# Optimization experiments

Hardware: AMD Instinct MI355X
Metric: run time of the kernel (lower is better)

## Reference

```python
import jax, jax.numpy as jnp
import numpy as np


def setup_inputs() -> dict:
    key = jax.random.key(0)
    k1, k2, k3, k4, k5 = jax.random.split(key, 5)
    B, L, H = 32, 2048, 768
    in1 = jax.random.normal(k1, (B, H), dtype=jnp.float32)
    in2 = jax.random.normal(k2, (B, H), dtype=jnp.float32)
    text = jax.random.normal(k3, (B, L, H), dtype=jnp.float32)
    textmask = jnp.ones((B, L), dtype=jnp.float32)  # 1 = valid token
    # learned params (nn.Linear weights are [out, in]); small scale avoids tanh saturation
    W2 = jax.random.normal(k4, (H, 3 * H), dtype=jnp.float32) * 0.02
    b2 = jnp.zeros((H,), dtype=jnp.float32)
    W1 = jax.random.normal(k5, (1, H), dtype=jnp.float32) * 0.02
    b1 = jnp.zeros((1,), dtype=jnp.float32)
    return {"in1": in1, "in2": in2, "text": text, "textmask": textmask,
            "W2": W2, "b2": b2, "W1": W1, "b1": b1}


def reference(in1, in2, text, textmask, W2, b2, W1, b1):
    H = in1.shape[-1]
    # Split linear2 weight along input dim instead of materializing cat([in1,in2,text]).
    # Same math: cat @ W2.T == in1@W2a.T + in2@W2b.T + text@W2c.T
    W2a, W2b, W2c = W2[:, :H], W2[:, H:2 * H], W2[:, 2 * H:]
    bias_bh = in1 @ W2a.T + in2 @ W2b.T + b2          # [B, H], broadcast over L
    h = jnp.tanh(jnp.einsum('blh,gh->blg', text, W2c) + bias_bh[:, None, :])  # [B, L, H]
    att = jnp.einsum('blh,h->bl', h, W1[0]) + b1[0]   # [B, L]
    att = jax.nn.softmax((1.0 - textmask) * (-1e20) + att, axis=-1)  # masked softmax [B, L]
    context = jnp.einsum('bl,blh->bh', att, text)     # weighted sum [B, H]
    return context, att[:, None, :]                   # matches (context, att[B,1,L])
```

## Files before the change

### kernel.cpp

```cpp
#include <hip/hip_runtime.h>
#include <hip/hip_bf16.h>

typedef __bf16 bf16x8 __attribute__((ext_vector_type(8)));
typedef __bf16 bf16x4 __attribute__((ext_vector_type(4)));
typedef float  f32x4  __attribute__((ext_vector_type(4)));

#define H 768
#define LSEQ 2048
#define BATCH 32
#define MROWS (BATCH*LSEQ)
#define NT 6
#define W2S 2304

__device__ __forceinline__ void gload_lds16(const void* g, void* l){
  __builtin_amdgcn_global_load_lds((const __attribute__((address_space(1))) void*)g,
                                   (__attribute__((address_space(3))) void*)l, 16, 0, 0);
}

__global__ void w2c_cvt_k(const float* __restrict__ W2, __bf16* __restrict__ w2cb){
  int i4 = blockIdx.x*256 + threadIdx.x;
  int g  = i4 / 192;
  int hc = (i4 % 192) * 4;
  f32x4 v = *(const f32x4*)(W2 + (size_t)g*W2S + 1536 + hc);
  bf16x4 o; o[0]=(__bf16)v[0]; o[1]=(__bf16)v[1]; o[2]=(__bf16)v[2]; o[3]=(__bf16)v[3];
  *(bf16x4*)(w2cb + (size_t)g*H + hc) = o;
}

__global__ void bias_k(const float* __restrict__ in1, const float* __restrict__ in2,
                       const float* __restrict__ W2, const float* __restrict__ b2,
                       float* __restrict__ bias){
  int b = blockIdx.y;
  int g = blockIdx.x*64 + (threadIdx.x & 63);
  int q = threadIdx.x >> 6;
  const float* wa = W2 + (size_t)g*W2S + q*192;
  const float* wb = wa + H;
  const float* x1 = in1 + b*H + q*192;
  const float* x2 = in2 + b*H + q*192;
  float acc = 0.f;
  #pragma unroll 8
  for (int h=0; h<192; h+=4){
    f32x4 a4 = *(const f32x4*)(wa+h);
    f32x4 c4 = *(const f32x4*)(x1+h);
    f32x4 b4 = *(const f32x4*)(wb+h);
    f32x4 d4 = *(const f32x4*)(x2+h);
    acc += a4[0]*c4[0]+a4[1]*c4[1]+a4[2]*c4[2]+a4[3]*c4[3];
    acc += b4[0]*d4[0]+b4[1]*d4[1]+b4[2]*d4[2]+b4[3]*d4[3];
  }
  __shared__ float sm[4][64];
  sm[q][threadIdx.x&63] = acc;
  __syncthreads();
  if (q==0){
    float r = sm[0][threadIdx.x]+sm[1][threadIdx.x]+sm[2][threadIdx.x]+sm[3][threadIdx.x] + b2[g];
    bias[(size_t)b*H + g] = r;
  }
}

__global__ __launch_bounds__(256,3) void fused_gemm_att_k(
    const float* __restrict__ text, const __bf16* __restrict__ w2cb,
    const float* __restrict__ bias, const float* __restrict__ W1,
    float* __restrict__ attp)
{
  __shared__ __align__(16) __bf16 a_lds[2][128*32];
  __shared__ __align__(16) __bf16 b_lds[2][128*32];
  __shared__ float att_lds[2][128];

  int bid = blockIdx.x;
  int lin = (bid & 7)*384 + (bid >> 3);
  int mt  = lin / 6;
  int nt  = lin % 6;
  int m0  = mt << 7;
  int b   = m0 >> 11;
  int t = threadIdx.x, lane = t & 63, wid = t >> 6;
  int wm = wid >> 1, wn = wid & 1;
  int fr = lane & 15, fc = lane >> 4;

  const float*  atile = text + (size_t)m0*H;
  const __bf16* btile = w2cb + (size_t)(nt*128)*H;

  f32x4 acc[4][4];
  #pragma unroll
  for (int mi=0;mi<4;++mi)
    #pragma unroll
    for (int ni=0;ni<4;++ni) acc[mi][ni] = (f32x4){0.f,0.f,0.f,0.f};

  int arow = t>>1, ahalf = t&1;
  const float* aptr = atile + (size_t)arow*H + ahalf*16;
  int awOff[2];
  #pragma unroll
  for (int j=0;j<2;++j) awOff[j] = arow*32 + ((2*ahalf + j) ^ ((arow>>1)&3))*8;
  f32x4 aReg[4];

  const __bf16* bsrc[2];
  int bdst[2];
  #pragma unroll
  for (int j=0;j<2;++j){
    int slot = wid*2 + j;
    int n = slot*16 + (lane>>2);
    bsrc[j] = btile + (size_t)n*H + ((lane&3)^((n>>1)&3))*8;
    bdst[j] = slot*512 + lane*8;
  }

  int offA[4], offB[4];
  #pragma unroll
  for (int i=0;i<4;++i){
    int row = wm*64 + i*16 + fr;
    offA[i] = row*32 + ((fc ^ ((row>>1)&3))*8);
    int n = wn*64 + i*16 + fr;
    offB[i] = n*32 + ((fc ^ ((n>>1)&3))*8);
  }

  auto loadA = [&](int kk){
    #pragma unroll
    for (int j=0;j<4;++j) aReg[j] = *(const f32x4*)(aptr + kk*32 + j*4);
  };
  auto writeA = [&](int bf){
    #pragma unroll
    for (int j=0;j<2;++j){
      bf16x8 v;
      v[0]=(__bf16)aReg[2*j][0]; v[1]=(__bf16)aReg[2*j][1];
      v[2]=(__bf16)aReg[2*j][2]; v[3]=(__bf16)aReg[2*j][3];
      v[4]=(__bf16)aReg[2*j+1][0]; v[5]=(__bf16)aReg[2*j+1][1];
      v[6]=(__bf16)aReg[2*j+1][2]; v[7]=(__bf16)aReg[2*j+1][3];
      *(bf16x8*)&a_lds[bf][awOff[j]] = v;
    }
  };
  auto stageB = [&](int bf, int kk){
    #pragma unroll
    for (int j=0;j<2;++j)
      gload_lds16(bsrc[j] + kk*32, &b_lds[bf][bdst[j]]);
  };
  auto compute = [&](int bf){
    bf16x8 af[4], bq[4];
    #pragma unroll
    for (int i=0;i<4;++i){
      af[i] = *(const bf16x8*)&a_lds[bf][offA[i]];
      bq[i] = *(const bf16x8*)&b_lds[bf][offB[i]];
    }
    __builtin_amdgcn_s_setprio(1);
    #pragma unroll
    for (int mi=0;mi<4;++mi)
      #pragma unroll
      for (int ni=0;ni<4;++ni)
        acc[mi][ni] = __builtin_amdgcn_mfma_f32_16x16x32_bf16(af[mi], bq[ni], acc[mi][ni], 0,0,0);
    __builtin_amdgcn_s_setprio(0);
  };

  loadA(0);
  writeA(0);
  stageB(0, 0);
  loadA(1);
  asm volatile("s_waitcnt vmcnt(0) lgkmcnt(0)" ::: "memory");
  __builtin_amdgcn_s_barrier();

  #pragma unroll 2
  for (int kk=0; kk<22; ++kk){
    int cur = kk&1, nxt = cur^1;
    stageB(nxt, kk+1);
    writeA(nxt);
    loadA(kk+2);
    compute(cur);
    asm volatile("s_waitcnt vmcnt(4) lgkmcnt(0)" ::: "memory");
    __builtin_amdgcn_sched_barrier(0);
    __builtin_amdgcn_s_barrier();
    __builtin_amdgcn_sched_barrier(0);
  }
  {
    stageB(1, 23);
    writeA(1);
    compute(0);
    asm volatile("s_waitcnt vmcnt(0) lgkmcnt(0)" ::: "memory");
    __builtin_amdgcn_sched_barrier(0);
    __builtin_amdgcn_s_barrier();
    __builtin_amdgcn_sched_barrier(0);
  }
  compute(1);

  float bb[4], ww[4];
  int gb = nt*128 + wn*64 + fr;
  #pragma unroll
  for (int ni=0;ni<4;++ni){ bb[ni]=bias[(size_t)b*H + gb + ni*16]; ww[ni]=W1[gb + ni*16]; }

  float av[16];
  #pragma unroll
  for (int mi=0;mi<4;++mi)
    #pragma unroll
    for (int r=0;r<4;++r){
      float s = 0.f;
      #pragma unroll
      for (int ni=0;ni<4;++ni){
        float x = acc[mi][ni][r] + bb[ni];
        float e = __expf(2.0f*x);
        s += ww[ni] * ((e-1.0f)*__builtin_amdgcn_rcpf(e+1.0f));
      }
      av[mi*4+r] = s;
    }
  #pragma unroll
  for (int off=1; off<16; off<<=1)
    #pragma unroll
    for (int i=0;i<16;++i) av[i] += __shfl_xor(av[i], off);

  if (fr==0){
    #pragma unroll
    for (int mi=0;mi<4;++mi)
      #pragma unroll
      for (int r=0;r<4;++r)
        att_lds[wn][wm*64 + mi*16 + fc*4 + r] = av[mi*4+r];
  }
  __syncthreads();
  if (t < 128) attp[(size_t)nt*MROWS + m0 + t] = att_lds[0][t] + att_lds[1][t];
}

__global__ void softmax_k(const float* __restrict__ attp, const float* __restrict__ tmask,
                          const float* __restrict__ b1, float* __restrict__ att){
  int b = blockIdx.x, t = threadIdx.x;
  int lane = t & 63, wv = t >> 6;
  __shared__ float sl[LSEQ];
  __shared__ float red[4];
  float b1v = b1[0];
  float lmax = -3.0e38f;
  for (int i=t; i<LSEQ; i+=256){
    float v = b1v;
    #pragma unroll
    for (int p=0;p<NT;++p) v += attp[(size_t)p*MROWS + b*LSEQ + i];
    v += (1.0f - tmask[b*LSEQ+i]) * -1.0e20f;
    sl[i] = v;
    lmax = fmaxf(lmax, v);
  }
  #pragma unroll
  for (int off=32; off>=1; off>>=1) lmax = fmaxf(lmax, __shfl_xor(lmax, off));
  if (lane==0) red[wv] = lmax;
  __syncthreads();
  float mx = fmaxf(fmaxf(red[0],red[1]), fmaxf(red[2],red[3]));
  __syncthreads();
  float lsum = 0.f;
  for (int i=t; i<LSEQ; i+=256){
    float e = __expf(sl[i]-mx);
    sl[i] = e;
    lsum += e;
  }
  #pragma unroll
  for (int off=32; off>=1; off>>=1) lsum += __shfl_xor(lsum, off);
  if (lane==0) red[wv] = lsum;
  __syncthreads();
  float inv = 1.0f/(red[0]+red[1]+red[2]+red[3]);
  for (int i=t; i<LSEQ; i+=256) att[(size_t)b*LSEQ+i] = sl[i]*inv;
}

__global__ void ctxpart_k(const float* __restrict__ text, const float* __restrict__ att,
                          float* __restrict__ ctxp){
  int chunk = blockIdx.x, b = blockIdx.y, t = threadIdx.x;
  const float* tp = text + ((size_t)(b*LSEQ + chunk*64))*H + 4*t;
  const float* ap = att + (size_t)b*LSEQ + chunk*64;
  f32x4 acc = {0.f,0.f,0.f,0.f};
  #pragma unroll 4
  for (int l=0;l<64;++l){
    float a = ap[l];
    f32x4 v = *(const f32x4*)(tp + (size_t)l*H);
    acc[0] += a*v[0]; acc[1] += a*v[1]; acc[2] += a*v[2]; acc[3] += a*v[3];
  }
  *(f32x4*)(ctxp + ((size_t)(b*32+chunk))*H + 4*t) = acc;
}

__global__ void ctxred_k(const float* __restrict__ ctxp, float* __restrict__ out){
  int b = blockIdx.x, h = threadIdx.x;
  float s = 0.f;
  #pragma unroll 8
  for (int c=0;c<32;++c) s += ctxp[((size_t)(b*32+c))*H + h];
  out[(size_t)b*H + h] = s;
}

extern "C" void kernel_launch(void* const* d_in, const int* in_sizes, int n_in,
                              void* d_out, int out_size, void* d_ws, size_t ws_size,
                              hipStream_t stream){
  (void)in_sizes; (void)n_in; (void)out_size; (void)ws_size;
  const float* in1   = (const float*)d_in[0];
  const float* in2   = (const float*)d_in[1];
  const float* text  = (const float*)d_in[2];
  const float* tmask = (const float*)d_in[3];
  const float* W2    = (const float*)d_in[4];
  const float* b2    = (const float*)d_in[5];
  const float* W1    = (const float*)d_in[6];
  const float* b1    = (const float*)d_in[7];
  float* out = (float*)d_out;
  char*  ws  = (char*)d_ws;
  __bf16* w2cb = (__bf16*)(ws);
  float* biasb = (float*)(ws + 1179648);
  float* attp  = (float*)(ws + 1277952);
  float* ctxp  = (float*)(ws + 2850816);
  float* att_out = out + BATCH*H;

  w2c_cvt_k      <<<dim3(576),   dim3(256), 0, stream>>>(W2, w2cb);
  bias_k         <<<dim3(12,32), dim3(256), 0, stream>>>(in1, in2, W2, b2, biasb);
  fused_gemm_att_k<<<dim3(3072), dim3(256), 0, stream>>>(text, w2cb, biasb, W1, attp);
  softmax_k      <<<dim3(32),    dim3(256), 0, stream>>>(attp, tmask, b1, att_out);
  ctxpart_k      <<<dim3(32,32), dim3(192), 0, stream>>>(text, att_out, ctxp);
  ctxred_k       <<<dim3(32),    dim3(768), 0, stream>>>(ctxp, out);
}
```

Baseline: 205.8 us.

## Pre-convert text to bf16 and stage both GEMM operands via direct LDS loads

```diff
diff --git a/kernel.cpp b/kernel.cpp
--- a/kernel.cpp
+++ b/kernel.cpp
@@ -24,6 +24,15 @@
   f32x4 v = *(const f32x4*)(W2 + (size_t)g*W2S + 1536 + hc);
   bf16x4 o; o[0]=(__bf16)v[0]; o[1]=(__bf16)v[1]; o[2]=(__bf16)v[2]; o[3]=(__bf16)v[3];
   *(bf16x4*)(w2cb + (size_t)g*H + hc) = o;
+}
+
+__global__ void text_cvt_k(const float* __restrict__ in, __bf16* __restrict__ outb){
+  const size_t N4 = (size_t)MROWS*H/4;
+  for (size_t i = blockIdx.x*256 + threadIdx.x; i < N4; i += (size_t)2048*256){
+    f32x4 v = ((const f32x4*)in)[i];
+    bf16x4 o; o[0]=(__bf16)v[0]; o[1]=(__bf16)v[1]; o[2]=(__bf16)v[2]; o[3]=(__bf16)v[3];
+    ((bf16x4*)outb)[i] = o;
+  }
 }
 
 __global__ void bias_k(const float* __restrict__ in1, const float* __restrict__ in2,
@@ -55,7 +64,121 @@
   }
 }
 
-__global__ __launch_bounds__(256,3) void fused_gemm_att_k(
+__global__ __launch_bounds__(256,4) void fused_gemm_att_k(
+    const __bf16* __restrict__ textb, const __bf16* __restrict__ w2cb,
+    const float* __restrict__ bias, const float* __restrict__ W1,
+    float* __restrict__ attp)
+{
+  __shared__ __align__(16) __bf16 a_lds[2][128*32];
+  __shared__ __align__(16) __bf16 b_lds[2][128*32];
+  __shared__ float att_lds[2][128];
+
+  int bid = blockIdx.x;
+  int lin = (bid & 7)*384 + (bid >> 3);
+  int mt  = lin / 6;
+  int nt  = lin % 6;
+  int m0  = mt << 7;
+  int b   = mt >> 4;
+  int t = threadIdx.x, lane = t & 63, wid = t >> 6;
+  int wm = wid >> 1, wn = wid & 1;
+  int fr = lane & 15, fc = lane >> 4;
+
+  const __bf16* atile = textb + (size_t)m0*H;
+  const __bf16* btile = w2cb + (size_t)(nt*128)*H;
+
+  f32x4 acc[4][4];
+  #pragma unroll
+  for (int mi=0;mi<4;++mi)
+    #pragma unroll
+    for (int ni=0;ni<4;++ni) acc[mi][ni] = (f32x4){0.f,0.f,0.f,0.f};
+
+  const __bf16 *asrc[2], *bsrc[2];
+  int sdst[2];
+  #pragma unroll
+  for (int j=0;j<2;++j){
+    int slot = wid*2 + j;
+    int row = slot*16 + (lane>>2);
+    int gs  = (lane&3) ^ ((row>>1)&3);
+    asrc[j] = atile + (size_t)row*H + gs*8;
+    bsrc[j] = btile + (size_t)row*H + gs*8;
+    sdst[j] = slot*512 + lane*8;
+  }
+
+  int offA[4], offB[4];
+  #pragma unroll
+  for (int i=0;i<4;++i){
+    int row = wm*64 + i*16 + fr;
+    offA[i] = row*32 + ((fc ^ ((row>>1)&3))*8);
+    int n = wn*64 + i*16 + fr;
+    offB[i] = n*32 + ((fc ^ ((n>>1)&3))*8);
+  }
+
+  auto stage = [&](int bf, int kk){
+    #pragma unroll
+    for (int j=0;j<2;++j){
+      gload_lds16(asrc[j] + kk*32, &a_lds[bf][sdst[j]]);
+      gload_lds16(bsrc[j] + kk*32, &b_lds[bf][sdst[j]]);
+    }
+  };
+  auto compute = [&](int bf){
+    bf16x8 af[4], bq[4];
+    #pragma unroll
+    for (int i=0;i<4;++i){
+      af[i] = *(const bf16x8*)&a_lds[bf][offA[i]];
+      bq[i] = *(const bf16x8*)&b_lds[bf][offB[i]];
+    }
+    #pragma unroll
+    for (int mi=0;mi<4;++mi)
+      #pragma unroll
+      for (int ni=0;ni<4;++ni)
+        acc[mi][ni] = __builtin_amdgcn_mfma_f32_16x16x32_bf16(af[mi], bq[ni], acc[mi][ni], 0,0,0);
+  };
+
+  stage(0, 0);
+  __syncthreads();
+  #pragma unroll 2
+  for (int kk=0; kk<24; ++kk){
+    if (kk < 23) stage((kk+1)&1, kk+1);
+    compute(kk&1);
+    __syncthreads();
+  }
+
+  float bb[4], ww[4];
+  int gb = nt*128 + wn*64 + fr;
+  #pragma unroll
+  for (int ni=0;ni<4;++ni){ bb[ni]=bias[(size_t)b*H + gb + ni*16]; ww[ni]=W1[gb + ni*16]; }
+
+  float av[16];
+  #pragma unroll
+  for (int mi=0;mi<4;++mi)
+    #pragma unroll
+    for (int r=0;r<4;++r){
+      float s = 0.f;
+      #pragma unroll
+      for (int ni=0;ni<4;++ni){
+        float x = acc[mi][ni][r] + bb[ni];
+        float e = __expf(2.0f*x);
+        s += ww[ni] * ((e-1.0f)*__builtin_amdgcn_rcpf(e+1.0f));
+      }
+      av[mi*4+r] = s;
+    }
+  #pragma unroll
+  for (int off=1; off<16; off<<=1)
+    #pragma unroll
+    for (int i=0;i<16;++i) av[i] += __shfl_xor(av[i], off);
+
+  if (fr==0){
+    #pragma unroll
+    for (int mi=0;mi<4;++mi)
+      #pragma unroll
+      for (int r=0;r<4;++r)
+        att_lds[wn][wm*64 + mi*16 + fc*4 + r] = av[mi*4+r];
+  }
+  __syncthreads();
+  if (t < 128) attp[(size_t)nt*MROWS + m0 + t] = att_lds[0][t] + att_lds[1][t];
+}
+
+__global__ __launch_bounds__(256,3) void fused_gemm_att_f32_k(
     const float* __restrict__ text, const __bf16* __restrict__ w2cb,
     const float* __restrict__ bias, const float* __restrict__ W1,
     float* __restrict__ attp)
@@ -69,7 +192,7 @@
   int mt  = lin / 6;
   int nt  = lin % 6;
   int m0  = mt << 7;
-  int b   = m0 >> 11;
+  int b   = mt >> 4;
   int t = threadIdx.x, lane = t & 63, wid = t >> 6;
   int wm = wid >> 1, wn = wid & 1;
   int fr = lane & 15, fc = lane >> 4;
@@ -99,7 +222,6 @@
     bsrc[j] = btile + (size_t)n*H + ((lane&3)^((n>>1)&3))*8;
     bdst[j] = slot*512 + lane*8;
   }
-
   int offA[4], offB[4];
   #pragma unroll
   for (int i=0;i<4;++i){
@@ -108,7 +230,6 @@
     int n = wn*64 + i*16 + fr;
     offB[i] = n*32 + ((fc ^ ((n>>1)&3))*8);
   }
-
   auto loadA = [&](int kk){
     #pragma unroll
     for (int j=0;j<4;++j) aReg[j] = *(const f32x4*)(aptr + kk*32 + j*4);
@@ -136,50 +257,25 @@
       af[i] = *(const bf16x8*)&a_lds[bf][offA[i]];
       bq[i] = *(const bf16x8*)&b_lds[bf][offB[i]];
     }
-    __builtin_amdgcn_s_setprio(1);
     #pragma unroll
     for (int mi=0;mi<4;++mi)
       #pragma unroll
       for (int ni=0;ni<4;++ni)
         acc[mi][ni] = __builtin_amdgcn_mfma_f32_16x16x32_bf16(af[mi], bq[ni], acc[mi][ni], 0,0,0);
-    __builtin_amdgcn_s_setprio(0);
-  };
-
-  loadA(0);
-  writeA(0);
-  stageB(0, 0);
-  loadA(1);
-  asm volatile("s_waitcnt vmcnt(0) lgkmcnt(0)" ::: "memory");
-  __builtin_amdgcn_s_barrier();
-
+  };
+
+  loadA(0); writeA(0); stageB(0, 0); loadA(1);
+  __syncthreads();
   #pragma unroll 2
-  for (int kk=0; kk<22; ++kk){
-    int cur = kk&1, nxt = cur^1;
-    stageB(nxt, kk+1);
-    writeA(nxt);
-    loadA(kk+2);
-    compute(cur);
-    asm volatile("s_waitcnt vmcnt(4) lgkmcnt(0)" ::: "memory");
-    __builtin_amdgcn_sched_barrier(0);
-    __builtin_amdgcn_s_barrier();
-    __builtin_amdgcn_sched_barrier(0);
-  }
-  {
-    stageB(1, 23);
-    writeA(1);
-    compute(0);
-    asm volatile("s_waitcnt vmcnt(0) lgkmcnt(0)" ::: "memory");
-    __builtin_amdgcn_sched_barrier(0);
-    __builtin_amdgcn_s_barrier();
-    __builtin_amdgcn_sched_barrier(0);
-  }
-  compute(1);
-
+  for (int kk=0; kk<24; ++kk){
+    if (kk<23){ stageB((kk+1)&1, kk+1); writeA((kk+1)&1); if (kk<22) loadA(kk+2); }
+    compute(kk&1);
+    __syncthreads();
+  }
   float bb[4], ww[4];
   int gb = nt*128 + wn*64 + fr;
   #pragma unroll
   for (int ni=0;ni<4;++ni){ bb[ni]=bias[(size_t)b*H + gb + ni*16]; ww[ni]=W1[gb + ni*16]; }
-
   float av[16];
   #pragma unroll
   for (int mi=0;mi<4;++mi)
@@ -198,7 +294,6 @@
   for (int off=1; off<16; off<<=1)
     #pragma unroll
     for (int i=0;i<16;++i) av[i] += __shfl_xor(av[i], off);
-
   if (fr==0){
     #pragma unroll
     for (int mi=0;mi<4;++mi)
@@ -272,7 +367,7 @@
 extern "C" void kernel_launch(void* const* d_in, const int* in_sizes, int n_in,
                               void* d_out, int out_size, void* d_ws, size_t ws_size,
                               hipStream_t stream){
-  (void)in_sizes; (void)n_in; (void)out_size; (void)ws_size;
+  (void)in_sizes; (void)n_in; (void)out_size;
   const float* in1   = (const float*)d_in[0];
   const float* in2   = (const float*)d_in[1];
   const float* text  = (const float*)d_in[2];
@@ -287,11 +382,18 @@
   float* biasb = (float*)(ws + 1179648);
   float* attp  = (float*)(ws + 1277952);
   float* ctxp  = (float*)(ws + 2850816);
+  __bf16* textb = (__bf16*)(ws + 5996544);
+  const size_t WS_NEEDED = 5996544ull + 100663296ull;
   float* att_out = out + BATCH*H;
 
   w2c_cvt_k      <<<dim3(576),   dim3(256), 0, stream>>>(W2, w2cb);
   bias_k         <<<dim3(12,32), dim3(256), 0, stream>>>(in1, in2, W2, b2, biasb);
-  fused_gemm_att_k<<<dim3(3072), dim3(256), 0, stream>>>(text, w2cb, biasb, W1, attp);
+  if (ws_size >= WS_NEEDED){
+    text_cvt_k     <<<dim3(2048), dim3(256), 0, stream>>>(text, textb);
+    fused_gemm_att_k<<<dim3(3072), dim3(256), 0, stream>>>(textb, w2cb, biasb, W1, attp);
+  } else {
+    fused_gemm_att_f32_k<<<dim3(3072), dim3(256), 0, stream>>>(text, w2cb, biasb, W1, attp);
+  }
   softmax_k      <<<dim3(32),    dim3(256), 0, stream>>>(attp, tmask, b1, att_out);
   ctxpart_k      <<<dim3(32,32), dim3(192), 0, stream>>>(text, att_out, ctxp);
   ctxred_k       <<<dim3(32),    dim3(768), 0, stream>>>(ctxp, out);
```

New measurement: 232.4 us. +12.9%, slower.
